# Optimization experiments

Measured on AMD Instinct MI355X. Metric: run time of the kernel, lower is better.

Reference implementation:

```python
import jax, jax.numpy as jnp
import numpy as np

HIDDEN = 128
GATF = 128
HEADS = 4
N_M, N_D = 8192, 6144
N = N_M + N_D


def gcn_conv(x, edges, ew, W, b):
    """PyG GCNConv with edge weights and self-loops (weight 1)."""
    n = x.shape[0]
    loop = jnp.arange(n, dtype=edges.dtype)
    src = jnp.concatenate([edges[0], loop])
    dst = jnp.concatenate([edges[1], loop])
    w = jnp.concatenate([ew, jnp.ones((n,), x.dtype)])
    deg = jax.ops.segment_sum(w, dst, num_segments=n)
    dinv = jnp.where(deg > 0, jax.lax.rsqrt(deg), 0.0)
    norm = dinv[src] * w * dinv[dst]                 # [E+n]
    h = x @ W                                        # [n, F]
    msg = h[src] * norm[:, None]                     # gather + scale
    return jax.ops.segment_sum(msg, dst, num_segments=n) + b


def gatv2_conv(x, edge_index, Wl, Wr, att, bias):
    """PyG GATv2Conv, concat=False (head mean), self-loops, slope 0.2."""
    n = x.shape[0]
    H, C = att.shape
    loop = jnp.arange(n, dtype=edge_index.dtype)
    src = jnp.concatenate([edge_index[0], loop])
    dst = jnp.concatenate([edge_index[1], loop])
    xl = (x @ Wl).reshape(n, H, C)
    xr = (x @ Wr).reshape(n, H, C)
    e = jax.nn.leaky_relu(xl[src] + xr[dst], 0.2)    # [E, H, C]
    logits = jnp.einsum('ehc,hc->eh', e, att)        # [E, H]
    mx = jax.ops.segment_max(logits, dst, num_segments=n)
    ex = jnp.exp(logits - mx[dst])
    denom = jax.ops.segment_sum(ex, dst, num_segments=n)
    alpha = ex / denom[dst]                          # segment softmax
    out = jax.ops.segment_sum(xl[src] * alpha[:, :, None], dst, num_segments=n)
    return out.mean(axis=1) + bias


def setup_inputs() -> dict:
    key = jax.random.key(0)
    ks = jax.random.split(key, 24)
    f32 = jnp.float32
    def glorot(k, shape):
        fan = shape[0] + shape[-1] if len(shape) == 2 else int(np.prod(shape))
        s = np.sqrt(2.0 / fan).astype(np.float32)
        return jax.random.normal(k, shape, f32) * s
    inp = {
        'mm_f': jax.random.normal(ks[0], (N_M, HIDDEN), f32),
        'd_s_feat': jax.random.normal(ks[1], (N_D, HIDDEN), f32),
        'ms_mat': jax.random.uniform(ks[2], (N_M, N_M), f32),
        'ds_mat': jax.random.uniform(ks[3], (N_D, N_D), f32),
        'mm_edges': jax.random.randint(ks[4], (2, 131072), 0, N_M, jnp.int32),
        'dd_edges': jax.random.randint(ks[5], (2, 98304), 0, N_D, jnp.int32),
        'edge_index': jax.random.randint(ks[6], (2, 229376), 0, N, jnp.int32),
        # GCN params
        'W_m1': glorot(ks[7], (HIDDEN, HIDDEN)), 'b_m1': jnp.zeros((HIDDEN,), f32),
        'W_m2': glorot(ks[8], (HIDDEN, HIDDEN)), 'b_m2': jnp.zeros((HIDDEN,), f32),
        'W_d1': glorot(ks[9], (HIDDEN, HIDDEN)), 'b_d1': jnp.zeros((HIDDEN,), f32),
        'W_d2': glorot(ks[10], (HIDDEN, HIDDEN)), 'b_d2': jnp.zeros((HIDDEN,), f32),
        # GATv2 layer 1: GATF -> GATF//2 per head, HEADS heads
        'Wl1': glorot(ks[11], (GATF, HEADS * (GATF // 2))),
        'Wr1': glorot(ks[12], (GATF, HEADS * (GATF // 2))),
        'att1': glorot(ks[13], (HEADS, GATF // 2)),
        'bias1': jnp.zeros((GATF // 2,), f32),
        # GATv2 layer 2: GATF//2 -> GATF//4 per head
        'Wl2': glorot(ks[14], (GATF // 2, HEADS * (GATF // 4))),
        'Wr2': glorot(ks[15], (GATF // 2, HEADS * (GATF // 4))),
        'att2': glorot(ks[16], (HEADS, GATF // 4)),
        'bias2': jnp.zeros((GATF // 4,), f32),
        # JK linear: (GATF + GATF//2 + GATF//4) -> HIDDEN
        'W_jk': glorot(ks[17], (GATF + GATF // 2 + GATF // 4, HIDDEN)),
        'b_jk': jnp.zeros((HIDDEN,), f32),
    }
    return inp


def reference(mm_f, d_s_feat, ms_mat, ds_mat, mm_edges, dd_edges, edge_index,
              W_m1, b_m1, W_m2, b_m2, W_d1, b_d1, W_d2, b_d2,
              Wl1, Wr1, att1, bias1, Wl2, Wr2, att2, bias2, W_jk, b_jk):
    # GCN_GAT feature extraction
    ew_m = ms_mat[mm_edges[0], mm_edges[1]]
    ew_d = ds_mat[dd_edges[0], dd_edges[1]]
    m1 = jax.nn.relu(gcn_conv(mm_f, mm_edges, ew_m, W_m1, b_m1))
    m2 = gcn_conv(m1, mm_edges, ew_m, W_m2, b_m2)
    d1 = jax.nn.relu(gcn_conv(d_s_feat, dd_edges, ew_d, W_d1, b_d1))
    d2 = gcn_conv(d1, dd_edges, ew_d, W_d2, b_d2)
    x0 = jnp.concatenate([jax.nn.relu(m2), jax.nn.relu(d2)], axis=0)  # [N, GATF]
    # GATv2 stack with JumpingKnowledge('cat')
    x1 = jax.nn.elu(gatv2_conv(x0, edge_index, Wl1, Wr1, att1, bias1))
    x2 = gatv2_conv(x1, edge_index, Wl2, Wr2, att2, bias2)
    xjk = jnp.concatenate([x0, x1, x2], axis=-1)
    return xjk @ W_jk + b_jk
```

## Files before the change

kernel.cpp:

```cpp
#include <hip/hip_runtime.h>
#include <math.h>

#define NM   8192
#define NDD  6144
#define NN   14336
#define EMM  131072
#define EDD  98304
#define E2   (EMM + EDD)
#define EGAT 229376

typedef __attribute__((ext_vector_type(8))) short bf16x8;
typedef __attribute__((ext_vector_type(4))) float f32x4;

static __device__ __forceinline__ ushort f2bf(float x) {
  unsigned u = __float_as_uint(x);
  unsigned r = (u + 0x7FFFu + ((u >> 16) & 1u)) >> 16;
  return (ushort)r;
}
static __device__ __forceinline__ float bf2f(ushort h) {
  return __uint_as_float(((unsigned)h) << 16);
}
static __device__ __forceinline__ void split_store(float x, ushort* ph, ushort* pl) {
  ushort hh = f2bf(x);
  *ph = hh;
  *pl = f2bf(x - bf2f(hh));
}

__global__ __launch_bounds__(256) void init_kern(
    float* __restrict__ deg, int* __restrict__ cg, int* __restrict__ ca) {
  int i = blockIdx.x * 256 + threadIdx.x;
  if (i < NN) { deg[i] = 1.0f; cg[i] = 0; ca[i] = 0; }
}

__global__ __launch_bounds__(256) void hist_kern(
    const float* __restrict__ ms, const float* __restrict__ dsm,
    const int* __restrict__ mmE, const int* __restrict__ ddE,
    const int* __restrict__ eidx,
    float* __restrict__ ew, float* __restrict__ deg,
    int* __restrict__ cnt_gcn, int* __restrict__ cnt_gat) {
  int e = blockIdx.x * 256 + threadIdx.x;
  if (e < E2) {
    float w; int dg;
    if (e < EMM) {
      int s = mmE[e], d = mmE[EMM + e];
      w = ms[(size_t)s * NM + d]; dg = d;
    } else {
      int e2 = e - EMM;
      int s = ddE[e2], d = ddE[EDD + e2];
      w = dsm[(size_t)s * NDD + d]; dg = d + NM;
    }
    ew[e] = w;
    atomicAdd(deg + dg, w);
    atomicAdd(cnt_gcn + dg, 1);
  } else {
    int e2 = e - E2;
    if (e2 < EGAT) atomicAdd(cnt_gat + eidx[EGAT + e2], 1);
  }
}

__global__ __launch_bounds__(256) void make_dinv(float* deg) {
  int i = blockIdx.x * 256 + threadIdx.x;
  if (i < NN) deg[i] = 1.0f / sqrtf(deg[i]);
}

__global__ __launch_bounds__(1024) void scan_kern(
    const int* __restrict__ cntA, int* rsA, int* curA,
    const int* __restrict__ cntB, int* rsB, int* curB) {
  const int* cnt = blockIdx.x ? cntB : cntA;
  int* rs  = blockIdx.x ? rsB : rsA;
  int* cur = blockIdx.x ? curB : curA;
  __shared__ int buf[1024];
  __shared__ int carry;
  int t = threadIdx.x;
  if (t == 0) carry = 0;
  __syncthreads();
  for (int base = 0; base < NN; base += 1024) {
    int v = cnt[base + t];
    buf[t] = v;
    __syncthreads();
    for (int off = 1; off < 1024; off <<= 1) {
      int x = (t >= off) ? buf[t - off] : 0;
      __syncthreads();
      buf[t] += x;
      __syncthreads();
    }
    int excl = carry + buf[t] - v;
    rs[base + t] = excl;
    cur[base + t] = excl;
    int total = buf[1023];
    __syncthreads();
    if (t == 0) carry += total;
    __syncthreads();
  }
  if (t == 0) rs[NN] = carry;
}

__global__ __launch_bounds__(256) void fill_kern(
    const int* __restrict__ mmE, const int* __restrict__ ddE,
    const int* __restrict__ eidx,
    const float* __restrict__ ew, const float* __restrict__ dinv,
    int* __restrict__ cur_gcn, int* __restrict__ csrc, float* __restrict__ cw,
    int* __restrict__ cur_gat, int* __restrict__ gsrc) {
  int e = blockIdx.x * 256 + threadIdx.x;
  if (e < E2) {
    int sg, dg;
    if (e < EMM) { sg = mmE[e]; dg = mmE[EMM + e]; }
    else { int e2 = e - EMM; sg = ddE[e2] + NM; dg = ddE[EDD + e2] + NM; }
    float nrm = dinv[sg] * ew[e] * dinv[dg];
    int pos = atomicAdd(cur_gcn + dg, 1);
    csrc[pos] = sg; cw[pos] = nrm;
  } else {
    int e2 = e - E2;
    if (e2 < EGAT) {
      int src = eidx[e2], dst = eidx[EGAT + e2];
      int pos = atomicAdd(cur_gat + dst, 1);
      gsrc[pos] = src;
    }
  }
}

__global__ __launch_bounds__(256) void wsplit_kern(
    const float* W0, const float* W1, const float* W2, const float* W3,
    const float* W4, const float* W5, const float* W6, const float* W7,
    const float* W8, ushort* __restrict__ dst) {
  int idx = blockIdx.x * 256 + threadIdx.x;
  const int cum[9] = {16384, 32768, 49152, 65536, 98304, 131072, 139264, 147456, 176128};
  const int Ks[9]  = {128, 128, 128, 128, 128, 128, 64, 64, 224};
  const int Ns[9]  = {128, 128, 128, 128, 256, 256, 128, 128, 128};
  const float* Ws[9] = {W0, W1, W2, W3, W4, W5, W6, W7, W8};
  int seg = 0;
  while (idx >= cum[seg]) seg++;
  int base = seg ? cum[seg - 1] : 0;
  int S = cum[seg] - base;
  int o = idx - base;
  int K = Ks[seg], Nn = Ns[seg];
  int n = o / K, k = o - n * K;
  float x = Ws[seg][(size_t)k * Nn + n];
  split_store(x, dst + 2 * (size_t)base + o, dst + 2 * (size_t)base + S + o);
}

__global__ __launch_bounds__(256) void split_in_kern(
    const float* __restrict__ a, const float* __restrict__ b,
    ushort* __restrict__ oh, ushort* __restrict__ ol) {
  int idx = blockIdx.x * 256 + threadIdx.x;
  float x = (idx < NM * 128) ? a[idx] : b[idx - NM * 128];
  split_store(x, oh + idx, ol + idx);
}

template <int KT, int NT, bool BIAS>
__global__ __launch_bounds__(256) void gemm_kern(
    const ushort* __restrict__ Ah, const ushort* __restrict__ Al,
    int lda, int aoff,
    const ushort* __restrict__ WhA, const ushort* __restrict__ WlA,
    const ushort* __restrict__ WhB, const ushort* __restrict__ WlB,
    int splitRow,
    const float* __restrict__ bias,
    float* __restrict__ C, int ldc) {
  constexpr int NS = KT / 32;
  int w = threadIdx.x >> 6, lane = threadIdx.x & 63;
  int m0 = blockIdx.x * 64 + w * 16;
  int n0 = blockIdx.y * 16;
  const ushort* Wh = (m0 < splitRow) ? WhA : WhB;
  const ushort* Wl = (m0 < splitRow) ? WlA : WlB;
  int lm = lane & 15, kg = lane >> 4;
  bf16x8 wh[NS], wl[NS];
  const ushort* wp = Wh + (size_t)(n0 + lm) * KT + kg * 8;
  const ushort* wq = Wl + (size_t)(n0 + lm) * KT + kg * 8;
#pragma unroll
  for (int s = 0; s < NS; s++) {
    wh[s] = *reinterpret_cast<const bf16x8*>(wp + s * 32);
    wl[s] = *reinterpret_cast<const bf16x8*>(wq + s * 32);
  }
  const ushort* ap = Ah + (size_t)(m0 + lm) * lda + aoff + kg * 8;
  const ushort* aq = Al + (size_t)(m0 + lm) * lda + aoff + kg * 8;
  f32x4 acc = {0.f, 0.f, 0.f, 0.f};
#pragma unroll
  for (int s = 0; s < NS; s++) {
    bf16x8 ah = *reinterpret_cast<const bf16x8*>(ap + s * 32);
    bf16x8 al = *reinterpret_cast<const bf16x8*>(aq + s * 32);
    acc = __builtin_amdgcn_mfma_f32_16x16x32_bf16(ah, wh[s], acc, 0, 0, 0);
    acc = __builtin_amdgcn_mfma_f32_16x16x32_bf16(al, wh[s], acc, 0, 0, 0);
    acc = __builtin_amdgcn_mfma_f32_16x16x32_bf16(ah, wl[s], acc, 0, 0, 0);
  }
#pragma unroll
  for (int r = 0; r < 4; r++) {
    float v = acc[r];
    if (BIAS) v += bias[n0 + lm];
    C[(size_t)(m0 + kg * 4 + r) * ldc + n0 + lm] = v;
  }
}

__global__ __launch_bounds__(256) void gcn_gather_kern(
    const float* __restrict__ h, const float* __restrict__ dinv,
    const float* __restrict__ ba, const float* __restrict__ bb,
    const int* __restrict__ rs, const int* __restrict__ csrc,
    const float* __restrict__ cw,
    ushort* __restrict__ outh, ushort* __restrict__ outl, int ldo) {
  int n = blockIdx.x * 2 + (threadIdx.x >> 7);
  int f = threadIdx.x & 127;
  float di = dinv[n];
  const float* b = (n < NM) ? ba : bb;
  float acc = b[f] + h[(size_t)n * 128 + f] * di * di;
  int p = rs[n], p1 = rs[n + 1];
  for (; p + 1 < p1; p += 2) {
    int s0 = csrc[p], s1 = csrc[p + 1];
    float w0 = cw[p], w1 = cw[p + 1];
    acc += h[(size_t)s0 * 128 + f] * w0;
    acc += h[(size_t)s1 * 128 + f] * w1;
  }
  if (p < p1) acc += h[(size_t)csrc[p] * 128 + f] * cw[p];
  acc = fmaxf(acc, 0.f);
  size_t o = (size_t)n * ldo + f;
  split_store(acc, outh + o, outl + o);
}

template <int C, bool ELU>
__global__ __launch_bounds__(4 * C) void gat_gather_kern(
    const float* __restrict__ xl, const float* __restrict__ xr,
    const float* __restrict__ att, const float* __restrict__ bias,
    const int* __restrict__ rs, const int* __restrict__ gsrc,
    ushort* __restrict__ outh, ushort* __restrict__ outl, int ldo, int off) {
  constexpr int HC = 4 * C;
  constexpr int VPL = C / 16;
  constexpr int WAVES = HC / 64;
  constexpr int CAP = 512;
  __shared__ float xr_s[HC], att_s[HC];
  __shared__ float lgb[CAP][4];
  __shared__ float part[WAVES][HC];
  __shared__ float den_s[4];
  int n = blockIdx.x;
  int tid = threadIdx.x, w = tid >> 6, lane = tid & 63;
  xr_s[tid] = xr[(size_t)n * HC + tid];
  att_s[tid] = att[tid];
  int p0 = rs[n];
  int deg = rs[n + 1] - p0;
  int tot = deg + 1;
  if (tot > CAP) tot = CAP;
  __syncthreads();
  int h0 = lane >> 4;
  for (int ee = w; ee < tot; ee += WAVES) {
    int src = (ee < deg) ? gsrc[p0 + ee] : n;
    const float* xlr = xl + (size_t)src * HC + lane * VPL;
    float xv[VPL];
    if constexpr (VPL == 4) {
      float4 t4 = *reinterpret_cast<const float4*>(xlr);
      xv[0] = t4.x; xv[1] = t4.y; xv[2] = t4.z; xv[3] = t4.w;
    } else {
      float2 t2 = *reinterpret_cast<const float2*>(xlr);
      xv[0] = t2.x; xv[1] = t2.y;
    }
    float s = 0.f;
#pragma unroll
    for (int v = 0; v < VPL; v++) {
      int f = lane * VPL + v;
      float t = xv[v] + xr_s[f];
      t = (t > 0.f) ? t : 0.2f * t;
      s += t * att_s[f];
    }
    s += __shfl_xor(s, 1); s += __shfl_xor(s, 2);
    s += __shfl_xor(s, 4); s += __shfl_xor(s, 8);
    if ((lane & 15) == 0) lgb[ee][h0] = s;
  }
  __syncthreads();
  if (tid < 4) {
    float m = -1e30f;
    for (int ee = 0; ee < tot; ee++) m = fmaxf(m, lgb[ee][tid]);
    float d = 0.f;
    for (int ee = 0; ee < tot; ee++) {
      float x = __expf(lgb[ee][tid] - m);
      lgb[ee][tid] = x; d += x;
    }
    den_s[tid] = d;
  }
  __syncthreads();
  float a[VPL];
#pragma unroll
  for (int v = 0; v < VPL; v++) a[v] = 0.f;
  for (int ee = w; ee < tot; ee += WAVES) {
    int src = (ee < deg) ? gsrc[p0 + ee] : n;
    const float* xlr = xl + (size_t)src * HC + lane * VPL;
    float exv = lgb[ee][h0];
    if constexpr (VPL == 4) {
      float4 t4 = *reinterpret_cast<const float4*>(xlr);
      a[0] += t4.x * exv; a[1] += t4.y * exv;
      a[2] += t4.z * exv; a[3] += t4.w * exv;
    } else {
      float2 t2 = *reinterpret_cast<const float2*>(xlr);
      a[0] += t2.x * exv; a[1] += t2.y * exv;
    }
  }
#pragma unroll
  for (int v = 0; v < VPL; v++) part[w][lane * VPL + v] = a[v];
  __syncthreads();
  float sum = 0.f;
#pragma unroll
  for (int w2 = 0; w2 < WAVES; w2++) sum += part[w2][tid];
  sum /= den_s[tid / C];
  __syncthreads();
  part[0][tid] = sum;
  __syncthreads();
  if (tid < C) {
    float vv = 0.25f * (part[0][tid] + part[0][C + tid] +
                        part[0][2 * C + tid] + part[0][3 * C + tid]) + bias[tid];
    if (ELU) vv = (vv > 0.f) ? vv : (__expf(vv) - 1.f);
    size_t o = (size_t)n * ldo + off + tid;
    split_store(vv, outh + o, outl + o);
  }
}

extern "C" void kernel_launch(void* const* d_in, const int* in_sizes, int n_in,
                              void* d_out, int out_size, void* d_ws, size_t ws_size,
                              hipStream_t stream) {
  const float* mm_f = (const float*)d_in[0];
  const float* d_sf = (const float*)d_in[1];
  const float* msM  = (const float*)d_in[2];
  const float* dsM  = (const float*)d_in[3];
  const int*   mmE  = (const int*)d_in[4];
  const int*   ddE  = (const int*)d_in[5];
  const int*   eidx = (const int*)d_in[6];
  const float* W_m1 = (const float*)d_in[7];  const float* b_m1 = (const float*)d_in[8];
  const float* W_m2 = (const float*)d_in[9];  const float* b_m2 = (const float*)d_in[10];
  const float* W_d1 = (const float*)d_in[11]; const float* b_d1 = (const float*)d_in[12];
  const float* W_d2 = (const float*)d_in[13]; const float* b_d2 = (const float*)d_in[14];
  const float* Wl1  = (const float*)d_in[15]; const float* Wr1  = (const float*)d_in[16];
  const float* att1 = (const float*)d_in[17]; const float* bias1= (const float*)d_in[18];
  const float* Wl2  = (const float*)d_in[19]; const float* Wr2  = (const float*)d_in[20];
  const float* att2 = (const float*)d_in[21]; const float* bias2= (const float*)d_in[22];
  const float* W_jk = (const float*)d_in[23]; const float* b_jk = (const float*)d_in[24];
  float* out = (float*)d_out;

  float* ew   = (float*)d_ws;
  float* cw   = ew + E2;
  float* dinv = cw + E2;
  float* h    = dinv + NN;
  float* xl   = h + (size_t)NN * 128;
  float* xr   = xl + (size_t)NN * 256;
  ushort* us   = (ushort*)(xr + (size_t)NN * 256);
  ushort* inh  = us;
  ushort* inl  = inh + (size_t)NN * 128;
  ushort* m1h  = inl + (size_t)NN * 128;
  ushort* m1l  = m1h + (size_t)NN * 128;
  ushort* xjkh = m1l + (size_t)NN * 128;
  ushort* xjkl = xjkh + (size_t)NN * 224;
  ushort* wts  = xjkl + (size_t)NN * 224;
  int* ip      = (int*)(wts + 352256);
  int* cnt_gcn = ip;
  int* rs_gcn  = cnt_gcn + NN;
  int* cur_gcn = rs_gcn + NN + 1;
  int* cnt_gat = cur_gcn + NN;
  int* rs_gat  = cnt_gat + NN;
  int* cur_gat = rs_gat + NN + 1;
  int* csrc    = cur_gat + NN;
  int* gsrc    = csrc + E2;

  ushort* m1Wh = wts + 0;      ushort* m1Wl = wts + 16384;
  ushort* m2Wh = wts + 32768;  ushort* m2Wl = wts + 49152;
  ushort* d1Wh = wts + 65536;  ushort* d1Wl = wts + 81920;
  ushort* d2Wh = wts + 98304;  ushort* d2Wl = wts + 114688;
  ushort* l1Wh = wts + 131072; ushort* l1Wl = wts + 163840;
  ushort* r1Wh = wts + 196608; ushort* r1Wl = wts + 229376;
  ushort* l2Wh = wts + 262144; ushort* l2Wl = wts + 270336;
  ushort* r2Wh = wts + 278528; ushort* r2Wl = wts + 286720;
  ushort* jkWh = wts + 294912; ushort* jkWl = wts + 323584;

  const int BIG = 1 << 30;

  init_kern<<<(NN + 255) / 256, 256, 0, stream>>>(dinv, cnt_gcn, cnt_gat);
  hist_kern<<<(E2 + EGAT) / 256, 256, 0, stream>>>(
      msM, dsM, mmE, ddE, eidx, ew, dinv, cnt_gcn, cnt_gat);
  make_dinv<<<(NN + 255) / 256, 256, 0, stream>>>(dinv);
  scan_kern<<<2, 1024, 0, stream>>>(cnt_gcn, rs_gcn, cur_gcn,
                                    cnt_gat, rs_gat, cur_gat);
  fill_kern<<<(E2 + EGAT) / 256, 256, 0, stream>>>(
      mmE, ddE, eidx, ew, dinv, cur_gcn, csrc, cw, cur_gat, gsrc);
  wsplit_kern<<<688, 256, 0, stream>>>(
      W_m1, W_m2, W_d1, W_d2, Wl1, Wr1, Wl2, Wr2, W_jk, wts);
  split_in_kern<<<NN * 128 / 256, 256, 0, stream>>>(mm_f, d_sf, inh, inl);

  gemm_kern<128, 128, false><<<dim3(NN / 64, 8), 256, 0, stream>>>(
      inh, inl, 128, 0, m1Wh, m1Wl, d1Wh, d1Wl, NM, nullptr, h, 128);
  gcn_gather_kern<<<NN / 2, 256, 0, stream>>>(
      h, dinv, b_m1, b_d1, rs_gcn, csrc, cw, m1h, m1l, 128);

  gemm_kern<128, 128, false><<<dim3(NN / 64, 8), 256, 0, stream>>>(
      m1h, m1l, 128, 0, m2Wh, m2Wl, d2Wh, d2Wl, NM, nullptr, h, 128);
  gcn_gather_kern<<<NN / 2, 256, 0, stream>>>(
      h, dinv, b_m2, b_d2, rs_gcn, csrc, cw, xjkh, xjkl, 224);

  gemm_kern<128, 256, false><<<dim3(NN / 64, 16), 256, 0, stream>>>(
      xjkh, xjkl, 224, 0, l1Wh, l1Wl, l1Wh, l1Wl, BIG, nullptr, xl, 256);
  gemm_kern<128, 256, false><<<dim3(NN / 64, 16), 256, 0, stream>>>(
      xjkh, xjkl, 224, 0, r1Wh, r1Wl, r1Wh, r1Wl, BIG, nullptr, xr, 256);
  gat_gather_kern<64, true><<<NN, 256, 0, stream>>>(
      xl, xr, att1, bias1, rs_gat, gsrc, xjkh, xjkl, 224, 128);

  gemm_kern<64, 128, false><<<dim3(NN / 64, 8), 256, 0, stream>>>(
      xjkh, xjkl, 224, 128, l2Wh, l2Wl, l2Wh, l2Wl, BIG, nullptr, xl, 128);
  gemm_kern<64, 128, false><<<dim3(NN / 64, 8), 256, 0, stream>>>(
      xjkh, xjkl, 224, 128, r2Wh, r2Wl, r2Wh, r2Wl, BIG, nullptr, xr, 128);
  gat_gather_kern<32, false><<<NN, 128, 0, stream>>>(
      xl, xr, att2, bias2, rs_gat, gsrc, xjkh, xjkl, 224, 192);

  gemm_kern<224, 128, true><<<dim3(NN / 64, 8), 256, 0, stream>>>(
      xjkh, xjkl, 224, 0, jkWh, jkWl, jkWh, jkWl, BIG, b_jk, out, 128);
}
```

Measured before the change: 783.3 us.

## Fuse prep kernels, warp-shuffle scan, online-softmax GAT, and full-N GEMM tiles

Merges the init, weight-split and input-split kernels into one prep kernel, and folds dinv computation into the scan kernel. The scan now uses wave shuffles instead of a shared-memory loop with many barriers. The GAT gather does a single pass with an online softmax, which removes the second gather over neighbours and the 512-entry logit cap. Each GEMM block now covers the full N dimension with the A tile held in registers, and the paired l/r projections share one launch. The trade-offs are fewer blocks per GEMM, more registers per thread, and weights read directly from global memory for every N tile.

```diff
diff --git a/kernel.cpp b/kernel.cpp
--- a/kernel.cpp
+++ b/kernel.cpp
@@ -8,6 +8,7 @@
 #define EDD  98304
 #define E2   (EMM + EDD)
 #define EGAT 229376
+#define WSEG 176128
 
 typedef __attribute__((ext_vector_type(8))) short bf16x8;
 typedef __attribute__((ext_vector_type(4))) float f32x4;
@@ -26,10 +27,36 @@
   *pl = f2bf(x - bf2f(hh));
 }
 
-__global__ __launch_bounds__(256) void init_kern(
-    float* __restrict__ deg, int* __restrict__ cg, int* __restrict__ ca) {
-  int i = blockIdx.x * 256 + threadIdx.x;
-  if (i < NN) { deg[i] = 1.0f; cg[i] = 0; ca[i] = 0; }
+__global__ __launch_bounds__(256) void prep_kern(
+    float* __restrict__ deg, int* __restrict__ cg, int* __restrict__ ca,
+    const float* W0, const float* W1, const float* W2, const float* W3,
+    const float* W4, const float* W5, const float* W6, const float* W7,
+    const float* W8, ushort* __restrict__ wdst,
+    const float* __restrict__ fa, const float* __restrict__ fb,
+    ushort* __restrict__ oh, ushort* __restrict__ ol) {
+  int idx = blockIdx.x * 256 + threadIdx.x;
+  if (idx < NN) { deg[idx] = 1.0f; cg[idx] = 0; ca[idx] = 0; }
+  int i1 = idx - NN;
+  if (i1 >= 0 && i1 < WSEG) {
+    const int cum[9] = {16384, 32768, 49152, 65536, 98304, 131072, 139264, 147456, 176128};
+    const int Ks[9]  = {128, 128, 128, 128, 128, 128, 64, 64, 224};
+    const int Ns[9]  = {128, 128, 128, 128, 256, 256, 128, 128, 128};
+    const float* Ws[9] = {W0, W1, W2, W3, W4, W5, W6, W7, W8};
+    int seg = 0;
+    while (i1 >= cum[seg]) seg++;
+    int base = seg ? cum[seg - 1] : 0;
+    int S = cum[seg] - base;
+    int o = i1 - base;
+    int K = Ks[seg], Nn = Ns[seg];
+    int n = o / K, k = o - n * K;
+    float x = Ws[seg][(size_t)k * Nn + n];
+    split_store(x, wdst + 2 * (size_t)base + o, wdst + 2 * (size_t)base + S + o);
+  }
+  int i2 = idx - (NN + WSEG);
+  if (i2 >= 0 && i2 < NN * 128) {
+    float x = (i2 < NM * 128) ? fa[i2] : fb[i2 - NM * 128];
+    split_store(x, oh + i2, ol + i2);
+  }
 }
 
 __global__ __launch_bounds__(256) void hist_kern(
@@ -58,41 +85,51 @@
   }
 }
 
-__global__ __launch_bounds__(256) void make_dinv(float* deg) {
-  int i = blockIdx.x * 256 + threadIdx.x;
-  if (i < NN) deg[i] = 1.0f / sqrtf(deg[i]);
-}
-
 __global__ __launch_bounds__(1024) void scan_kern(
     const int* __restrict__ cntA, int* rsA, int* curA,
-    const int* __restrict__ cntB, int* rsB, int* curB) {
+    const int* __restrict__ cntB, int* rsB, int* curB,
+    float* __restrict__ deg) {
   const int* cnt = blockIdx.x ? cntB : cntA;
   int* rs  = blockIdx.x ? rsB : rsA;
   int* cur = blockIdx.x ? curB : curA;
-  __shared__ int buf[1024];
-  __shared__ int carry;
-  int t = threadIdx.x;
-  if (t == 0) carry = 0;
+  for (int i = threadIdx.x; i < NN / 2; i += 1024) {
+    int j = blockIdx.x * (NN / 2) + i;
+    deg[j] = 1.0f / sqrtf(deg[j]);
+  }
+  __shared__ int wsum[16];
+  __shared__ int carry_s;
+  int t = threadIdx.x, w = t >> 6, lane = t & 63;
+  if (t == 0) carry_s = 0;
   __syncthreads();
   for (int base = 0; base < NN; base += 1024) {
     int v = cnt[base + t];
-    buf[t] = v;
+    int inc = v;
+#pragma unroll
+    for (int off = 1; off < 64; off <<= 1) {
+      int x = __shfl_up(inc, off);
+      if (lane >= off) inc += x;
+    }
+    if (lane == 63) wsum[w] = inc;
     __syncthreads();
-    for (int off = 1; off < 1024; off <<= 1) {
-      int x = (t >= off) ? buf[t - off] : 0;
-      __syncthreads();
-      buf[t] += x;
-      __syncthreads();
-    }
-    int excl = carry + buf[t] - v;
+    int carry = carry_s;
+    if (w == 0 && lane < 16) {
+      int s = wsum[lane];
+#pragma unroll
+      for (int off = 1; off < 16; off <<= 1) {
+        int x = __shfl_up(s, off);
+        if (lane >= off) s += x;
+      }
+      wsum[lane] = s;
+    }
+    __syncthreads();
+    int woff = w ? wsum[w - 1] : 0;
+    int excl = carry + woff + inc - v;
     rs[base + t] = excl;
     cur[base + t] = excl;
-    int total = buf[1023];
+    if (t == 0) carry_s = carry + wsum[15];
     __syncthreads();
-    if (t == 0) carry += total;
-    __syncthreads();
-  }
-  if (t == 0) rs[NN] = carry;
+  }
+  if (threadIdx.x == 0) rs[NN] = carry_s;
 }
 
 __global__ __launch_bounds__(256) void fill_kern(
@@ -119,35 +156,7 @@
   }
 }
 
-__global__ __launch_bounds__(256) void wsplit_kern(
-    const float* W0, const float* W1, const float* W2, const float* W3,
-    const float* W4, const float* W5, const float* W6, const float* W7,
-    const float* W8, ushort* __restrict__ dst) {
-  int idx = blockIdx.x * 256 + threadIdx.x;
-  const int cum[9] = {16384, 32768, 49152, 65536, 98304, 131072, 139264, 147456, 176128};
-  const int Ks[9]  = {128, 128, 128, 128, 128, 128, 64, 64, 224};
-  const int Ns[9]  = {128, 128, 128, 128, 256, 256, 128, 128, 128};
-  const float* Ws[9] = {W0, W1, W2, W3, W4, W5, W6, W7, W8};
-  int seg = 0;
-  while (idx >= cum[seg]) seg++;
-  int base = seg ? cum[seg - 1] : 0;
-  int S = cum[seg] - base;
-  int o = idx - base;
-  int K = Ks[seg], Nn = Ns[seg];
-  int n = o / K, k = o - n * K;
-  float x = Ws[seg][(size_t)k * Nn + n];
-  split_store(x, dst + 2 * (size_t)base + o, dst + 2 * (size_t)base + S + o);
-}
-
-__global__ __launch_bounds__(256) void split_in_kern(
-    const float* __restrict__ a, const float* __restrict__ b,
-    ushort* __restrict__ oh, ushort* __restrict__ ol) {
-  int idx = blockIdx.x * 256 + threadIdx.x;
-  float x = (idx < NM * 128) ? a[idx] : b[idx - NM * 128];
-  split_store(x, oh + idx, ol + idx);
-}
-
-template <int KT, int NT, bool BIAS>
+template <int KT, int NT, bool BIAS, bool DUAL>
 __global__ __launch_bounds__(256) void gemm_kern(
     const ushort* __restrict__ Ah, const ushort* __restrict__ Al,
     int lda, int aoff,
@@ -155,38 +164,49 @@
     const ushort* __restrict__ WhB, const ushort* __restrict__ WlB,
     int splitRow,
     const float* __restrict__ bias,
-    float* __restrict__ C, int ldc) {
+    float* __restrict__ Ca, float* __restrict__ Cb, int ldc) {
   constexpr int NS = KT / 32;
   int w = threadIdx.x >> 6, lane = threadIdx.x & 63;
   int m0 = blockIdx.x * 64 + w * 16;
-  int n0 = blockIdx.y * 16;
-  const ushort* Wh = (m0 < splitRow) ? WhA : WhB;
-  const ushort* Wl = (m0 < splitRow) ? WlA : WlB;
+  const ushort* Wh; const ushort* Wl; float* C;
+  if (DUAL) {
+    Wh = blockIdx.y ? WhB : WhA;
+    Wl = blockIdx.y ? WlB : WlA;
+    C  = blockIdx.y ? Cb : Ca;
+  } else {
+    Wh = (m0 < splitRow) ? WhA : WhB;
+    Wl = (m0 < splitRow) ? WlA : WlB;
+    C  = Ca;
+  }
   int lm = lane & 15, kg = lane >> 4;
-  bf16x8 wh[NS], wl[NS];
-  const ushort* wp = Wh + (size_t)(n0 + lm) * KT + kg * 8;
-  const ushort* wq = Wl + (size_t)(n0 + lm) * KT + kg * 8;
-#pragma unroll
-  for (int s = 0; s < NS; s++) {
-    wh[s] = *reinterpret_cast<const bf16x8*>(wp + s * 32);
-    wl[s] = *reinterpret_cast<const bf16x8*>(wq + s * 32);
-  }
+  bf16x8 ah[NS], al[NS];
   const ushort* ap = Ah + (size_t)(m0 + lm) * lda + aoff + kg * 8;
   const ushort* aq = Al + (size_t)(m0 + lm) * lda + aoff + kg * 8;
-  f32x4 acc = {0.f, 0.f, 0.f, 0.f};
 #pragma unroll
   for (int s = 0; s < NS; s++) {
-    bf16x8 ah = *reinterpret_cast<const bf16x8*>(ap + s * 32);
-    bf16x8 al = *reinterpret_cast<const bf16x8*>(aq + s * 32);
-    acc = __builtin_amdgcn_mfma_f32_16x16x32_bf16(ah, wh[s], acc, 0, 0, 0);
-    acc = __builtin_amdgcn_mfma_f32_16x16x32_bf16(al, wh[s], acc, 0, 0, 0);
-    acc = __builtin_amdgcn_mfma_f32_16x16x32_bf16(ah, wl[s], acc, 0, 0, 0);
-  }
-#pragma unroll
-  for (int r = 0; r < 4; r++) {
-    float v = acc[r];
-    if (BIAS) v += bias[n0 + lm];
-    C[(size_t)(m0 + kg * 4 + r) * ldc + n0 + lm] = v;
+    ah[s] = *reinterpret_cast<const bf16x8*>(ap + s * 32);
+    al[s] = *reinterpret_cast<const bf16x8*>(aq + s * 32);
+  }
+#pragma unroll
+  for (int nb = 0; nb < NT / 16; nb++) {
+    int n0 = nb * 16;
+    const ushort* wp = Wh + (size_t)(n0 + lm) * KT + kg * 8;
+    const ushort* wq = Wl + (size_t)(n0 + lm) * KT + kg * 8;
+    f32x4 acc = {0.f, 0.f, 0.f, 0.f};
+#pragma unroll
+    for (int s = 0; s < NS; s++) {
+      bf16x8 wh = *reinterpret_cast<const bf16x8*>(wp + s * 32);
+      bf16x8 wl = *reinterpret_cast<const bf16x8*>(wq + s * 32);
+      acc = __builtin_amdgcn_mfma_f32_16x16x32_bf16(ah[s], wh, acc, 0, 0, 0);
+      acc = __builtin_amdgcn_mfma_f32_16x16x32_bf16(al[s], wh, acc, 0, 0, 0);
+      acc = __builtin_amdgcn_mfma_f32_16x16x32_bf16(ah[s], wl, acc, 0, 0, 0);
+    }
+#pragma unroll
+    for (int r = 0; r < 4; r++) {
+      float v = acc[r];
+      if (BIAS) v += bias[n0 + lm];
+      C[(size_t)(m0 + kg * 4 + r) * ldc + n0 + lm] = v;
+    }
   }
 }
 
@@ -223,11 +243,9 @@
   constexpr int HC = 4 * C;
   constexpr int VPL = C / 16;
   constexpr int WAVES = HC / 64;
-  constexpr int CAP = 512;
   __shared__ float xr_s[HC], att_s[HC];
-  __shared__ float lgb[CAP][4];
-  __shared__ float part[WAVES][HC];
-  __shared__ float den_s[4];
+  __shared__ float aws[WAVES][HC];
+  __shared__ float mws[WAVES][4], dws[WAVES][4];
   int n = blockIdx.x;
   int tid = threadIdx.x, w = tid >> 6, lane = tid & 63;
   xr_s[tid] = xr[(size_t)n * HC + tid];
@@ -235,9 +253,17 @@
   int p0 = rs[n];
   int deg = rs[n + 1] - p0;
   int tot = deg + 1;
-  if (tot > CAP) tot = CAP;
   __syncthreads();
   int h0 = lane >> 4;
+  float xrv[VPL], atv[VPL];
+#pragma unroll
+  for (int v = 0; v < VPL; v++) {
+    xrv[v] = xr_s[lane * VPL + v];
+    atv[v] = att_s[lane * VPL + v];
+  }
+  float m = -1e30f, d = 0.f, a[VPL];
+#pragma unroll
+  for (int v = 0; v < VPL; v++) a[v] = 0.f;
   for (int ee = w; ee < tot; ee += WAVES) {
     int src = (ee < deg) ? gsrc[p0 + ee] : n;
     const float* xlr = xl + (size_t)src * HC + lane * VPL;
@@ -252,56 +278,42 @@
     float s = 0.f;
 #pragma unroll
     for (int v = 0; v < VPL; v++) {
-      int f = lane * VPL + v;
-      float t = xv[v] + xr_s[f];
+      float t = xv[v] + xrv[v];
       t = (t > 0.f) ? t : 0.2f * t;
-      s += t * att_s[f];
+      s += t * atv[v];
     }
     s += __shfl_xor(s, 1); s += __shfl_xor(s, 2);
     s += __shfl_xor(s, 4); s += __shfl_xor(s, 8);
-    if ((lane & 15) == 0) lgb[ee][h0] = s;
-  }
+    float mn = fmaxf(m, s);
+    float cs = __expf(m - mn);
+    float ps = __expf(s - mn);
+    d = d * cs + ps;
+#pragma unroll
+    for (int v = 0; v < VPL; v++) a[v] = a[v] * cs + ps * xv[v];
+    m = mn;
+  }
+#pragma unroll
+  for (int v = 0; v < VPL; v++) aws[w][lane * VPL + v] = a[v];
+  if ((lane & 15) == 0) { mws[w][h0] = m; dws[w][h0] = d; }
   __syncthreads();
-  if (tid < 4) {
-    float m = -1e30f;
-    for (int ee = 0; ee < tot; ee++) m = fmaxf(m, lgb[ee][tid]);
-    float d = 0.f;
-    for (int ee = 0; ee < tot; ee++) {
-      float x = __expf(lgb[ee][tid] - m);
-      lgb[ee][tid] = x; d += x;
-    }
-    den_s[tid] = d;
-  }
+  int hh = tid / C;
+  float M = mws[0][hh];
+#pragma unroll
+  for (int w2 = 1; w2 < WAVES; w2++) M = fmaxf(M, mws[w2][hh]);
+  float D = 0.f, A = 0.f;
+#pragma unroll
+  for (int w2 = 0; w2 < WAVES; w2++) {
+    float sc = __expf(mws[w2][hh] - M);
+    D += dws[w2][hh] * sc;
+    A += aws[w2][tid] * sc;
+  }
+  float sum = A / D;
   __syncthreads();
-  float a[VPL];
-#pragma unroll
-  for (int v = 0; v < VPL; v++) a[v] = 0.f;
-  for (int ee = w; ee < tot; ee += WAVES) {
-    int src = (ee < deg) ? gsrc[p0 + ee] : n;
-    const float* xlr = xl + (size_t)src * HC + lane * VPL;
-    float exv = lgb[ee][h0];
-    if constexpr (VPL == 4) {
-      float4 t4 = *reinterpret_cast<const float4*>(xlr);
-      a[0] += t4.x * exv; a[1] += t4.y * exv;
-      a[2] += t4.z * exv; a[3] += t4.w * exv;
-    } else {
-      float2 t2 = *reinterpret_cast<const float2*>(xlr);
-      a[0] += t2.x * exv; a[1] += t2.y * exv;
-    }
-  }
-#pragma unroll
-  for (int v = 0; v < VPL; v++) part[w][lane * VPL + v] = a[v];
-  __syncthreads();
-  float sum = 0.f;
-#pragma unroll
-  for (int w2 = 0; w2 < WAVES; w2++) sum += part[w2][tid];
-  sum /= den_s[tid / C];
-  __syncthreads();
-  part[0][tid] = sum;
+  aws[0][tid] = sum;
   __syncthreads();
   if (tid < C) {
-    float vv = 0.25f * (part[0][tid] + part[0][C + tid] +
-                        part[0][2 * C + tid] + part[0][3 * C + tid]) + bias[tid];
+    float vv = 0.25f * (aws[0][tid] + aws[0][C + tid] +
+                        aws[0][2 * C + tid] + aws[0][3 * C + tid]) + bias[tid];
     if (ELU) vv = (vv > 0.f) ? vv : (__expf(vv) - 1.f);
     size_t o = (size_t)n * ldo + off + tid;
     split_store(vv, outh + o, outl + o);
@@ -365,42 +377,37 @@
 
   const int BIG = 1 << 30;
 
-  init_kern<<<(NN + 255) / 256, 256, 0, stream>>>(dinv, cnt_gcn, cnt_gat);
+  prep_kern<<<(NN + WSEG + NN * 128) / 256, 256, 0, stream>>>(
+      dinv, cnt_gcn, cnt_gat,
+      W_m1, W_m2, W_d1, W_d2, Wl1, Wr1, Wl2, Wr2, W_jk, wts,
+      mm_f, d_sf, inh, inl);
   hist_kern<<<(E2 + EGAT) / 256, 256, 0, stream>>>(
       msM, dsM, mmE, ddE, eidx, ew, dinv, cnt_gcn, cnt_gat);
-  make_dinv<<<(NN + 255) / 256, 256, 0, stream>>>(dinv);
   scan_kern<<<2, 1024, 0, stream>>>(cnt_gcn, rs_gcn, cur_gcn,
-                                    cnt_gat, rs_gat, cur_gat);
+                                    cnt_gat, rs_gat, cur_gat, dinv);
   fill_kern<<<(E2 + EGAT) / 256, 256, 0, stream>>>(
       mmE, ddE, eidx, ew, dinv, cur_gcn, csrc, cw, cur_gat, gsrc);
-  wsplit_kern<<<688, 256, 0, stream>>>(
-      W_m1, W_m2, W_d1, W_d2, Wl1, Wr1, Wl2, Wr2, W_jk, wts);
-  split_in_kern<<<NN * 128 / 256, 256, 0, stream>>>(mm_f, d_sf, inh, inl);
-
-  gemm_kern<128, 128, false><<<dim3(NN / 64, 8), 256, 0, stream>>>(
-      inh, inl, 128, 0, m1Wh, m1Wl, d1Wh, d1Wl, NM, nullptr, h, 128);
+
+  gemm_kern<128, 128, false, false><<<dim3(NN / 64, 1), 256, 0, stream>>>(
+      inh, inl, 128, 0, m1Wh, m1Wl, d1Wh, d1Wl, NM, nullptr, h, nullptr, 128);
   gcn_gather_kern<<<NN / 2, 256, 0, stream>>>(
       h, dinv, b_m1, b_d1, rs_gcn, csrc, cw, m1h, m1l, 128);
 
-  gemm_kern<128, 128, false><<<dim3(NN / 64, 8), 256, 0, stream>>>(
-      m1h, m1l, 128, 0, m2Wh, m2Wl, d2Wh, d2Wl, NM, nullptr, h, 128);
+  gemm_kern<128, 128, false, false><<<dim3(NN / 64, 1), 256, 0, stream>>>(
+      m1h, m1l, 128, 0, m2Wh, m2Wl, d2Wh, d2Wl, NM, nullptr, h, nullptr, 128);
   gcn_gather_kern<<<NN / 2, 256, 0, stream>>>(
       h, dinv, b_m2, b_d2, rs_gcn, csrc, cw, xjkh, xjkl, 224);
 
-  gemm_kern<128, 256, false><<<dim3(NN / 64, 16), 256, 0, stream>>>(
-      xjkh, xjkl, 224, 0, l1Wh, l1Wl, l1Wh, l1Wl, BIG, nullptr, xl, 256);
-  gemm_kern<128, 256, false><<<dim3(NN / 64, 16), 256, 0, stream>>>(
-      xjkh, xjkl, 224, 0, r1Wh, r1Wl, r1Wh, r1Wl, BIG, nullptr, xr, 256);
+  gemm_kern<128, 256, false, true><<<dim3(NN / 64, 2), 256, 0, stream>>>(
+      xjkh, xjkl, 224, 0, l1Wh, l1Wl, r1Wh, r1Wl, 0, nullptr, xl, xr, 256);
   gat_gather_kern<64, true><<<NN, 256, 0, stream>>>(
       xl, xr, att1, bias1, rs_gat, gsrc, xjkh, xjkl, 224, 128);
 
-  gemm_kern<64, 128, false><<<dim3(NN / 64, 8), 256, 0, stream>>>(
-      xjkh, xjkl, 224, 128, l2Wh, l2Wl, l2Wh, l2Wl, BIG, nullptr, xl, 128);
-  gemm_kern<64, 128, false><<<dim3(NN / 64, 8), 256, 0, stream>>>(
-      xjkh, xjkl, 224, 128, r2Wh, r2Wl, r2Wh, r2Wl, BIG, nullptr, xr, 128);
+  gemm_kern<64, 128, false, true><<<dim3(NN / 64, 2), 256, 0, stream>>>(
+      xjkh, xjkl, 224, 128, l2Wh, l2Wl, r2Wh, r2Wl, 0, nullptr, xl, xr, 128);
   gat_gather_kern<32, false><<<NN, 128, 0, stream>>>(
       xl, xr, att2, bias2, rs_gat, gsrc, xjkh, xjkl, 224, 192);
 
-  gemm_kern<224, 128, true><<<dim3(NN / 64, 8), 256, 0, stream>>>(
-      xjkh, xjkl, 224, 0, jkWh, jkWl, jkWh, jkWl, BIG, b_jk, out, 128);
-}
+  gemm_kern<224, 128, true, false><<<dim3(NN / 64, 1), 256, 0, stream>>>(
+      xjkh, xjkl, 224, 0, jkWh, jkWl, jkWh, jkWl, BIG, b_jk, out, nullptr, 128);
+}
```

Measured after the change: 695.1 us. 1.13x faster.
